# Kernel optimization log

Measured on AMD Instinct MI355X. Metric: run time of the kernel, lower is better.

The kernel has to match this reference:

```python
import jax, jax.numpy as jnp
import numpy as np

NUM_HEADS = 16
D_IN = 1024
D_OUT = 64  # = D_IN // NUM_HEADS
N = 2048


def setup_inputs() -> dict:
    key = jax.random.key(0)
    kx, kq, kk, kv, ko = jax.random.split(key, 5)
    x = jax.random.normal(kx, (N, D_IN), dtype=jnp.float32)
    # per-head projection weights, stacked over heads (torch code keeps a
    # Python list of SelfAttention modules; stacking is the vectorized form)
    q_proj = jax.random.normal(kq, (NUM_HEADS, D_IN, D_OUT), dtype=jnp.float32)
    k_proj = jax.random.normal(kk, (NUM_HEADS, D_IN, D_OUT), dtype=jnp.float32)
    v_proj = jax.random.normal(kv, (NUM_HEADS, D_IN, D_OUT), dtype=jnp.float32)
    o_proj = jax.random.normal(ko, (D_IN, D_IN), dtype=jnp.float32)
    return {"x": x, "q_proj": q_proj, "k_proj": k_proj, "v_proj": v_proj, "o_proj": o_proj}


def reference(x, q_proj, k_proj, v_proj, o_proj):
    d_out = q_proj.shape[-1]
    # per-head projections: [H, N, E]
    q = jnp.einsum('nd,hde->hne', x, q_proj)
    k = jnp.einsum('nd,hde->hne', x, k_proj)
    v = jnp.einsum('nd,hde->hne', x, v_proj)
    # full NxN scores per head (matches the naive torch implementation's math)
    scores = jnp.einsum('hne,hme->hnm', q, k) / jnp.sqrt(jnp.float32(d_out))
    attn = jax.nn.softmax(scores, axis=-1)
    ctx = jnp.einsum('hnm,hme->hne', attn, v)
    # concat heads along the feature dim (head 0 first, as in torch.cat)
    h, n, e = ctx.shape
    out = jnp.transpose(ctx, (1, 0, 2)).reshape(n, h * e)
    return out @ o_proj
```

## Files before the change

### kernel.cpp

```cpp
#include <hip/hip_runtime.h>

#define H 16
#define N 2048
#define E 64
#define D 1024

typedef __attribute__((ext_vector_type(8))) short bf16x8;
typedef __attribute__((ext_vector_type(4))) float f32x4;

__device__ __forceinline__ float bf2f(unsigned short u) {
    union { unsigned int i; float f; } v;
    v.i = ((unsigned int)u) << 16;
    return v.f;
}
__device__ __forceinline__ unsigned short f2bf(float f) {
    unsigned int u = __float_as_uint(f);
    return (unsigned short)((u + 0x7fffu + ((u >> 16) & 1u)) >> 16);
}
#define MFMA(a, b, c) __builtin_amdgcn_mfma_f32_16x16x32_bf16(a, b, c, 0, 0, 0)

typedef __attribute__((address_space(3))) unsigned int lds_u32;
typedef const __attribute__((address_space(1))) unsigned int glb_u32;
__device__ __forceinline__ void dma16(const unsigned short* g, unsigned short* l) {
    __builtin_amdgcn_global_load_lds((glb_u32*)g, (lds_u32*)l, 16, 0, 0);
}

__device__ __forceinline__ int sw8(int row, int c)  { return row * 64  + ((c ^ (row & 7)) << 3); }
__device__ __forceinline__ int sw16(int row, int c) { return row * 128 + ((c ^ (row & 7)) << 3); }

__global__ __launch_bounds__(256) void convert_all_kernel(
    const float* __restrict__ x,
    const float* __restrict__ qw, const float* __restrict__ kw,
    const float* __restrict__ vw, const float* __restrict__ ow,
    unsigned short* __restrict__ xh, unsigned short* __restrict__ xl,
    unsigned short* __restrict__ wBh, unsigned short* __restrict__ wBl,
    unsigned short* __restrict__ wvt, unsigned short* __restrict__ woh)
{
    __shared__ float ts[64][65];
    const int b0 = blockIdx.x;
    const int t = threadIdx.x;
    if (b0 < 2048) {
        const int i = (b0 * 256 + t) * 4;
        const float4 v = *(const float4*)&x[i];
        ushort4 hh, ll;
        hh.x = f2bf(v.x); ll.x = f2bf(v.x - bf2f(hh.x));
        hh.y = f2bf(v.y); ll.y = f2bf(v.y - bf2f(hh.y));
        hh.z = f2bf(v.z); ll.z = f2bf(v.z - bf2f(hh.z));
        hh.w = f2bf(v.w); ll.w = f2bf(v.w - bf2f(hh.w));
        *(ushort4*)&xh[i] = hh;
        *(ushort4*)&xl[i] = ll;
        return;
    }
    const int b = b0 - 2048;
    const float* src;
    int rs, dt, orow0;
    bool has_lo;
    unsigned short *dh, *dl;
    if (b < 768) {
        const int which = b >> 8, r = b & 255, h = r >> 4;
        dt = r & 15;
        src = (which == 0 ? qw : which == 1 ? kw : vw) + ((size_t)h * D + dt * 64) * E;
        rs = E;
        if (which == 0)      { dh = wBh; dl = wBl; orow0 = h * 64;        has_lo = true; }
        else if (which == 1) { dh = wBh; dl = wBl; orow0 = 1024 + h * 64; has_lo = true; }
        else                 { dh = wvt; dl = wBl; orow0 = h * 64;        has_lo = false; }
    } else {
        const int r = b - 768, ct = r >> 4;
        dt = r & 15;
        src = ow + (size_t)(dt * 64) * D + ct * 64;
        rs = D;
        orow0 = ct * 64;
        dh = woh; dl = wBl; has_lo = false;
    }
    {
        const int row = t >> 2, cb = (t & 3) * 16;
        #pragma unroll
        for (int j = 0; j < 16; j += 4) {
            const float4 v = *(const float4*)&src[row * rs + cb + j];
            ts[row][cb + j + 0] = v.x;
            ts[row][cb + j + 1] = v.y;
            ts[row][cb + j + 2] = v.z;
            ts[row][cb + j + 3] = v.w;
        }
    }
    __syncthreads();
    {
        const int cl = t >> 2, dp = (t & 3) * 16;
        bf16x8 hv0, hv1, lv0, lv1;
        #pragma unroll
        for (int i = 0; i < 16; ++i) {
            const float f = ts[dp + i][cl];
            const unsigned short hh = f2bf(f);
            const unsigned short lo = f2bf(f - bf2f(hh));
            if (i < 8) { hv0[i] = (short)hh; lv0[i] = (short)lo; }
            else       { hv1[i - 8] = (short)hh; lv1[i - 8] = (short)lo; }
        }
        const size_t o = (size_t)(orow0 + cl) * D + dt * 64 + dp;
        *(bf16x8*)&dh[o] = hv0;
        *(bf16x8*)&dh[o + 8] = hv1;
        if (has_lo) {
            *(bf16x8*)&dl[o] = lv0;
            *(bf16x8*)&dl[o + 8] = lv1;
        }
    }
}

__global__ __launch_bounds__(256, 3) void qkv_kernel(
    const unsigned short* __restrict__ xh, const unsigned short* __restrict__ xl,
    const unsigned short* __restrict__ wBh, const unsigned short* __restrict__ wBl,
    const unsigned short* __restrict__ wvt,
    unsigned short* __restrict__ Qh, unsigned short* __restrict__ Ql,
    unsigned short* __restrict__ Kh, unsigned short* __restrict__ Kl,
    unsigned short* __restrict__ Vt)
{
    __shared__ unsigned short ash[128 * 64], asl[128 * 64];
    __shared__ unsigned short bsh[64 * 64], bsl[64 * 64];
    const int n0 = blockIdx.x * 128;
    const int ct0 = blockIdx.y;
    const int sec = ct0 >> 4;
    const int hh = ct0 & 15;
    const bool isv = (sec == 2);
    const unsigned short* Bh = isv ? wvt : wBh;
    const size_t brow0 = (sec == 1 ? 1024 : 0) + hh * 64;

    const int t = threadIdx.x;
    const int lane = t & 63, wvi = t >> 6, quad = lane >> 4, l15 = lane & 15;

    f32x4 acc[2][4];
    #pragma unroll
    for (int i = 0; i < 2; ++i)
        #pragma unroll
        for (int j = 0; j < 4; ++j) acc[i][j] = (f32x4){0.f, 0.f, 0.f, 0.f};

    for (int k0 = 0; k0 < D; k0 += 64) {
        __syncthreads();
        #pragma unroll
        for (int p = 0; p < 4; ++p) {
            const int row = p * 32 + wvi * 8 + (lane >> 3);
            const int lc = (lane & 7) ^ (row & 7);
            const int lo = p * 2048 + wvi * 512 + lane * 8;
            const size_t ga = (size_t)(n0 + row) * D + k0 + lc * 8;
            dma16(&xh[ga], &ash[lo]);
            if (!isv) dma16(&xl[ga], &asl[lo]);
        }
        #pragma unroll
        for (int p = 0; p < 2; ++p) {
            const int row = p * 32 + wvi * 8 + (lane >> 3);
            const int lc = (lane & 7) ^ (row & 7);
            const int lo = p * 2048 + wvi * 512 + lane * 8;
            const size_t gb = (brow0 + row) * D + k0 + lc * 8;
            dma16(&Bh[gb], &bsh[lo]);
            if (!isv) dma16(&wBl[gb], &bsl[lo]);
        }
        __syncthreads();

        #pragma unroll
        for (int kwi = 0; kwi < 2; ++kwi) {
            const int c = kwi * 4 + quad;
            bf16x8 ah[2], al[2], bh[4], bl[4];
            #pragma unroll
            for (int i = 0; i < 2; ++i) {
                ah[i] = *(const bf16x8*)&ash[sw8(wvi * 32 + i * 16 + l15, c)];
                if (!isv) al[i] = *(const bf16x8*)&asl[sw8(wvi * 32 + i * 16 + l15, c)];
            }
            #pragma unroll
            for (int j = 0; j < 4; ++j) {
                bh[j] = *(const bf16x8*)&bsh[sw8(j * 16 + l15, c)];
                if (!isv) bl[j] = *(const bf16x8*)&bsl[sw8(j * 16 + l15, c)];
            }
            #pragma unroll
            for (int i = 0; i < 2; ++i)
                #pragma unroll
                for (int j = 0; j < 4; ++j) {
                    acc[i][j] = MFMA(ah[i], bh[j], acc[i][j]);
                    if (!isv) {
                        acc[i][j] = MFMA(ah[i], bl[j], acc[i][j]);
                        acc[i][j] = MFMA(al[i], bh[j], acc[i][j]);
                    }
                }
        }
    }

    if (isv) {
        #pragma unroll
        for (int j = 0; j < 4; ++j) {
            const int e = j * 16 + l15;
            #pragma unroll
            for (int i = 0; i < 2; ++i) {
                const int nb = n0 + wvi * 32 + i * 16 + quad * 4;
                ushort4 pk;
                pk.x = f2bf(acc[i][j][0]);
                pk.y = f2bf(acc[i][j][1]);
                pk.z = f2bf(acc[i][j][2]);
                pk.w = f2bf(acc[i][j][3]);
                *(ushort4*)&Vt[((size_t)hh * 64 + e) * N + nb] = pk;
            }
        }
    } else {
        const float scale = (sec == 0) ? 0.125f : 1.0f;
        unsigned short* Oh = (sec == 0) ? Qh : Kh;
        unsigned short* Ol = (sec == 0) ? Ql : Kl;
        #pragma unroll
        for (int j = 0; j < 4; ++j) {
            const int e = j * 16 + l15;
            #pragma unroll
            for (int i = 0; i < 2; ++i)
                #pragma unroll
                for (int r = 0; r < 4; ++r) {
                    const int n = n0 + wvi * 32 + i * 16 + quad * 4 + r;
                    const float val = acc[i][j][r] * scale;
                    const unsigned short hv = f2bf(val);
                    Oh[((size_t)hh * N + n) * E + e] = hv;
                    Ol[((size_t)hh * N + n) * E + e] = f2bf(val - bf2f(hv));
                }
        }
    }
}

__global__ __launch_bounds__(256, 2) void attn_kernel(
    const unsigned short* __restrict__ Qh, const unsigned short* __restrict__ Ql,
    const unsigned short* __restrict__ Kh, const unsigned short* __restrict__ Kl,
    const unsigned short* __restrict__ Vt,
    unsigned short* __restrict__ Ch)
{
    __shared__ unsigned short ksh[128 * 64], ksl[128 * 64];
    __shared__ unsigned short vts[64 * 128];
    __shared__ unsigned short ps[4 * 16 * 136];
    const int r0 = blockIdx.x * 64, h = blockIdx.y;
    const int t = threadIdx.x, lane = t & 63, wvi = t >> 6, quad = lane >> 4, l15 = lane & 15;

    bf16x8 qfh[2], qfl[2];
    {
        const size_t base = ((size_t)h * N + r0 + wvi * 16 + l15) * E;
        #pragma unroll
        for (int kwi = 0; kwi < 2; ++kwi) {
            qfh[kwi] = *(const bf16x8*)&Qh[base + kwi * 32 + quad * 8];
            qfl[kwi] = *(const bf16x8*)&Ql[base + kwi * 32 + quad * 8];
        }
    }

    f32x4 oacc[4];
    #pragma unroll
    for (int ct = 0; ct < 4; ++ct) oacc[ct] = (f32x4){0.f, 0.f, 0.f, 0.f};
    float mrow[4] = {-1e30f, -1e30f, -1e30f, -1e30f};
    float lrow[4] = {0.f, 0.f, 0.f, 0.f};

    for (int m0 = 0; m0 < N; m0 += 128) {
        __syncthreads();
        #pragma unroll
        for (int p = 0; p < 4; ++p) {
            const int row = p * 32 + wvi * 8 + (lane >> 3);
            const int lc = (lane & 7) ^ (row & 7);
            const int lo = p * 2048 + wvi * 512 + lane * 8;
            const size_t gk = ((size_t)h * N + m0 + row) * E + lc * 8;
            dma16(&Kh[gk], &ksh[lo]);
            dma16(&Kl[gk], &ksl[lo]);
        }
        #pragma unroll
        for (int p = 0; p < 4; ++p) {
            const int row = p * 16 + wvi * 4 + (lane >> 4);
            const int lc = (lane & 15) ^ (row & 7);
            const int lo = p * 2048 + wvi * 512 + lane * 8;
            dma16(&Vt[((size_t)h * 64 + row) * N + m0 + lc * 8], &vts[lo]);
        }
        __syncthreads();

        f32x4 s[8];
        #pragma unroll
        for (int ct = 0; ct < 8; ++ct) s[ct] = (f32x4){0.f, 0.f, 0.f, 0.f};
        #pragma unroll
        for (int kwi = 0; kwi < 2; ++kwi) {
            const int c = kwi * 4 + quad;
            #pragma unroll
            for (int ct = 0; ct < 8; ++ct) {
                const bf16x8 bh = *(const bf16x8*)&ksh[sw8(ct * 16 + l15, c)];
                const bf16x8 bl = *(const bf16x8*)&ksl[sw8(ct * 16 + l15, c)];
                s[ct] = MFMA(qfh[kwi], bh, s[ct]);
                s[ct] = MFMA(qfh[kwi], bl, s[ct]);
                s[ct] = MFMA(qfl[kwi], bh, s[ct]);
            }
        }

        #pragma unroll
        for (int r = 0; r < 4; ++r) {
            float mx = s[0][r];
            #pragma unroll
            for (int ct = 1; ct < 8; ++ct) mx = fmaxf(mx, s[ct][r]);
            mx = fmaxf(mx, __shfl_xor(mx, 1));
            mx = fmaxf(mx, __shfl_xor(mx, 2));
            mx = fmaxf(mx, __shfl_xor(mx, 4));
            mx = fmaxf(mx, __shfl_xor(mx, 8));
            const float mn = fmaxf(mrow[r], mx);
            const float alpha = __expf(mrow[r] - mn);
            mrow[r] = mn;
            float sum = 0.f;
            #pragma unroll
            for (int ct = 0; ct < 8; ++ct) {
                const float p = __expf(s[ct][r] - mn);
                s[ct][r] = p;
                sum += p;
            }
            sum += __shfl_xor(sum, 1);
            sum += __shfl_xor(sum, 2);
            sum += __shfl_xor(sum, 4);
            sum += __shfl_xor(sum, 8);
            lrow[r] = lrow[r] * alpha + sum;
            #pragma unroll
            for (int ct = 0; ct < 4; ++ct) oacc[ct][r] *= alpha;
        }

        #pragma unroll
        for (int ct = 0; ct < 8; ++ct)
            #pragma unroll
            for (int r = 0; r < 4; ++r)
                ps[(wvi * 16 + quad * 4 + r) * 136 + ct * 16 + l15] = f2bf(s[ct][r]);

        #pragma unroll
        for (int kwi = 0; kwi < 4; ++kwi) {
            const bf16x8 pa = *(const bf16x8*)&ps[(wvi * 16 + l15) * 136 + kwi * 32 + quad * 8];
            #pragma unroll
            for (int ct = 0; ct < 4; ++ct) {
                const bf16x8 vb = *(const bf16x8*)&vts[sw16(ct * 16 + l15, kwi * 4 + quad)];
                oacc[ct] = MFMA(pa, vb, oacc[ct]);
            }
        }
    }

    #pragma unroll
    for (int r = 0; r < 4; ++r) {
        const float inv = 1.f / lrow[r];
        const int n = r0 + wvi * 16 + quad * 4 + r;
        #pragma unroll
        for (int ct = 0; ct < 4; ++ct)
            Ch[(size_t)n * D + h * 64 + ct * 16 + l15] = f2bf(oacc[ct][r] * inv);
    }
}

__global__ __launch_bounds__(256, 4) void out_proj_kernel(
    const unsigned short* __restrict__ Chh, const unsigned short* __restrict__ Wh,
    float* __restrict__ out)
{
    __shared__ unsigned short ash[64 * 64], bsh[64 * 64];
    const int n0 = blockIdx.x * 64, c0 = blockIdx.y * 64;
    const int t = threadIdx.x, lane = t & 63, wvi = t >> 6, quad = lane >> 4, l15 = lane & 15;

    f32x4 acc[4];
    #pragma unroll
    for (int j = 0; j < 4; ++j) acc[j] = (f32x4){0.f, 0.f, 0.f, 0.f};

    for (int k0 = 0; k0 < D; k0 += 64) {
        __syncthreads();
        #pragma unroll
        for (int p = 0; p < 2; ++p) {
            const int row = p * 32 + wvi * 8 + (lane >> 3);
            const int lc = (lane & 7) ^ (row & 7);
            const int lo = p * 2048 + wvi * 512 + lane * 8;
            dma16(&Chh[(size_t)(n0 + row) * D + k0 + lc * 8], &ash[lo]);
            dma16(&Wh[(size_t)(c0 + row) * D + k0 + lc * 8], &bsh[lo]);
        }
        __syncthreads();

        #pragma unroll
        for (int kwi = 0; kwi < 2; ++kwi) {
            const int c = kwi * 4 + quad;
            const bf16x8 ah = *(const bf16x8*)&ash[sw8(wvi * 16 + l15, c)];
            #pragma unroll
            for (int j = 0; j < 4; ++j) {
                const bf16x8 bh = *(const bf16x8*)&bsh[sw8(j * 16 + l15, c)];
                acc[j] = MFMA(ah, bh, acc[j]);
            }
        }
    }

    #pragma unroll
    for (int r = 0; r < 4; ++r) {
        const int n = n0 + wvi * 16 + quad * 4 + r;
        #pragma unroll
        for (int j = 0; j < 4; ++j)
            out[(size_t)n * D + c0 + j * 16 + l15] = acc[j][r];
    }
}

extern "C" void kernel_launch(void* const* d_in, const int* in_sizes, int n_in,
                              void* d_out, int out_size, void* d_ws, size_t ws_size,
                              hipStream_t stream) {
    const float* x  = (const float*)d_in[0];
    const float* qw = (const float*)d_in[1];
    const float* kw = (const float*)d_in[2];
    const float* vw = (const float*)d_in[3];
    const float* ow = (const float*)d_in[4];
    float* out = (float*)d_out;

    unsigned short* ws = (unsigned short*)d_ws;
    const size_t M1 = 1024 * 1024;
    unsigned short* wBh = ws;
    unsigned short* wBl = ws + 2 * M1;
    unsigned short* wvt = ws + 4 * M1;
    unsigned short* woh = ws + 5 * M1;
    unsigned short* xh  = ws + 6 * M1;
    unsigned short* xl  = ws + 8 * M1;
    unsigned short* Qh  = ws + 10 * M1;
    unsigned short* Ql  = ws + 12 * M1;
    unsigned short* Kh  = ws + 14 * M1;
    unsigned short* Kl  = ws + 16 * M1;
    unsigned short* Vt  = ws + 18 * M1;
    unsigned short* Ch  = xh;

    convert_all_kernel<<<3072, 256, 0, stream>>>(x, qw, kw, vw, ow,
                                                 xh, xl, wBh, wBl, wvt, woh);
    qkv_kernel<<<dim3(16, 48), 256, 0, stream>>>(xh, xl, wBh, wBl, wvt,
                                                 Qh, Ql, Kh, Kl, Vt);
    attn_kernel<<<dim3(32, 16), 256, 0, stream>>>(Qh, Ql, Kh, Kl, Vt, Ch);
    out_proj_kernel<<<dim3(32, 16), 256, 0, stream>>>(Ch, woh, out);
}
```

Measured before the change: 183.5 us.

## Split attention over KV halves with 128-row Q tiles, double-buffered K, and combine pass

```diff
diff --git a/kernel.cpp b/kernel.cpp
--- a/kernel.cpp
+++ b/kernel.cpp
@@ -27,6 +27,7 @@
 
 __device__ __forceinline__ int sw8(int row, int c)  { return row * 64  + ((c ^ (row & 7)) << 3); }
 __device__ __forceinline__ int sw16(int row, int c) { return row * 128 + ((c ^ (row & 7)) << 3); }
+__device__ __forceinline__ int swp(int row, int c)  { return row * 128 + ((c ^ (row & 15)) << 3); }
 
 __global__ __launch_bounds__(256) void convert_all_kernel(
     const float* __restrict__ x,
@@ -221,53 +222,68 @@
     const unsigned short* __restrict__ Qh, const unsigned short* __restrict__ Ql,
     const unsigned short* __restrict__ Kh, const unsigned short* __restrict__ Kl,
     const unsigned short* __restrict__ Vt,
-    unsigned short* __restrict__ Ch)
+    unsigned short* __restrict__ Op0, unsigned short* __restrict__ Op1,
+    float* __restrict__ mlp)
 {
-    __shared__ unsigned short ksh[128 * 64], ksl[128 * 64];
+    __shared__ unsigned short kbuf[2 * 16384];
     __shared__ unsigned short vts[64 * 128];
-    __shared__ unsigned short ps[4 * 16 * 136];
-    const int r0 = blockIdx.x * 64, h = blockIdx.y;
+    const int r0 = blockIdx.x * 128, h = blockIdx.y, split = blockIdx.z;
+    const int mb = split * 1024;
     const int t = threadIdx.x, lane = t & 63, wvi = t >> 6, quad = lane >> 4, l15 = lane & 15;
 
-    bf16x8 qfh[2], qfl[2];
-    {
-        const size_t base = ((size_t)h * N + r0 + wvi * 16 + l15) * E;
+    bf16x8 qfh[2][2], qfl[2][2];
+    #pragma unroll
+    for (int i = 0; i < 2; ++i) {
+        const size_t base = ((size_t)h * N + r0 + wvi * 32 + i * 16 + l15) * E;
         #pragma unroll
         for (int kwi = 0; kwi < 2; ++kwi) {
-            qfh[kwi] = *(const bf16x8*)&Qh[base + kwi * 32 + quad * 8];
-            qfl[kwi] = *(const bf16x8*)&Ql[base + kwi * 32 + quad * 8];
-        }
-    }
-
-    f32x4 oacc[4];
-    #pragma unroll
-    for (int ct = 0; ct < 4; ++ct) oacc[ct] = (f32x4){0.f, 0.f, 0.f, 0.f};
-    float mrow[4] = {-1e30f, -1e30f, -1e30f, -1e30f};
-    float lrow[4] = {0.f, 0.f, 0.f, 0.f};
-
-    for (int m0 = 0; m0 < N; m0 += 128) {
+            qfh[i][kwi] = *(const bf16x8*)&Qh[base + kwi * 32 + quad * 8];
+            qfl[i][kwi] = *(const bf16x8*)&Ql[base + kwi * 32 + quad * 8];
+        }
+    }
+
+    f32x4 oacc[2][4];
+    float mrow[2][4], lrow[2][4];
+    #pragma unroll
+    for (int i = 0; i < 2; ++i)
+        #pragma unroll
+        for (int j = 0; j < 4; ++j) {
+            oacc[i][j] = (f32x4){0.f, 0.f, 0.f, 0.f};
+            mrow[i][j] = -1e30f;
+            lrow[i][j] = 0.f;
+        }
+
+    #pragma unroll
+    for (int p = 0; p < 4; ++p) {
+        const int row = p * 32 + wvi * 8 + (lane >> 3);
+        const int lc = (lane & 7) ^ (row & 7);
+        const int lo = p * 2048 + wvi * 512 + lane * 8;
+        const size_t gk = ((size_t)h * N + mb + row) * E + lc * 8;
+        dma16(&Kh[gk], &kbuf[lo]);
+        dma16(&Kl[gk], &kbuf[8192 + lo]);
+    }
+
+    for (int it = 0; it < 8; ++it) {
+        const int cur = it & 1;
         __syncthreads();
-        #pragma unroll
-        for (int p = 0; p < 4; ++p) {
-            const int row = p * 32 + wvi * 8 + (lane >> 3);
-            const int lc = (lane & 7) ^ (row & 7);
-            const int lo = p * 2048 + wvi * 512 + lane * 8;
-            const size_t gk = ((size_t)h * N + m0 + row) * E + lc * 8;
-            dma16(&Kh[gk], &ksh[lo]);
-            dma16(&Kl[gk], &ksl[lo]);
-        }
+
         #pragma unroll
         for (int p = 0; p < 4; ++p) {
             const int row = p * 16 + wvi * 4 + (lane >> 4);
             const int lc = (lane & 15) ^ (row & 7);
             const int lo = p * 2048 + wvi * 512 + lane * 8;
-            dma16(&Vt[((size_t)h * 64 + row) * N + m0 + lc * 8], &vts[lo]);
-        }
-        __syncthreads();
-
-        f32x4 s[8];
-        #pragma unroll
-        for (int ct = 0; ct < 8; ++ct) s[ct] = (f32x4){0.f, 0.f, 0.f, 0.f};
+            dma16(&Vt[((size_t)h * 64 + row) * N + mb + it * 128 + lc * 8], &vts[lo]);
+        }
+
+        const unsigned short* ksh = &kbuf[cur * 16384];
+        const unsigned short* ksl = ksh + 8192;
+
+        f32x4 s[2][8];
+        #pragma unroll
+        for (int i = 0; i < 2; ++i)
+            #pragma unroll
+            for (int ct = 0; ct < 8; ++ct) s[i][ct] = (f32x4){0.f, 0.f, 0.f, 0.f};
+
         #pragma unroll
         for (int kwi = 0; kwi < 2; ++kwi) {
             const int c = kwi * 4 + quad;
@@ -275,64 +291,132 @@
             for (int ct = 0; ct < 8; ++ct) {
                 const bf16x8 bh = *(const bf16x8*)&ksh[sw8(ct * 16 + l15, c)];
                 const bf16x8 bl = *(const bf16x8*)&ksl[sw8(ct * 16 + l15, c)];
-                s[ct] = MFMA(qfh[kwi], bh, s[ct]);
-                s[ct] = MFMA(qfh[kwi], bl, s[ct]);
-                s[ct] = MFMA(qfl[kwi], bh, s[ct]);
-            }
-        }
-
+                #pragma unroll
+                for (int i = 0; i < 2; ++i) {
+                    s[i][ct] = MFMA(qfh[i][kwi], bh, s[i][ct]);
+                    s[i][ct] = MFMA(qfh[i][kwi], bl, s[i][ct]);
+                    s[i][ct] = MFMA(qfl[i][kwi], bh, s[i][ct]);
+                }
+            }
+        }
+
+        #pragma unroll
+        for (int i = 0; i < 2; ++i)
+            #pragma unroll
+            for (int r = 0; r < 4; ++r) {
+                float mx = s[i][0][r];
+                #pragma unroll
+                for (int ct = 1; ct < 8; ++ct) mx = fmaxf(mx, s[i][ct][r]);
+                mx = fmaxf(mx, __shfl_xor(mx, 1));
+                mx = fmaxf(mx, __shfl_xor(mx, 2));
+                mx = fmaxf(mx, __shfl_xor(mx, 4));
+                mx = fmaxf(mx, __shfl_xor(mx, 8));
+                const float mn = fmaxf(mrow[i][r], mx);
+                const float alpha = __expf(mrow[i][r] - mn);
+                mrow[i][r] = mn;
+                float sum = 0.f;
+                #pragma unroll
+                for (int ct = 0; ct < 8; ++ct) {
+                    const float p = __expf(s[i][ct][r] - mn);
+                    s[i][ct][r] = p;
+                    sum += p;
+                }
+                sum += __shfl_xor(sum, 1);
+                sum += __shfl_xor(sum, 2);
+                sum += __shfl_xor(sum, 4);
+                sum += __shfl_xor(sum, 8);
+                lrow[i][r] = lrow[i][r] * alpha + sum;
+                #pragma unroll
+                for (int ct = 0; ct < 4; ++ct) oacc[i][ct][r] *= alpha;
+            }
+
+        __syncthreads();
+
+        if (it < 7) {
+            #pragma unroll
+            for (int p = 0; p < 4; ++p) {
+                const int row = p * 32 + wvi * 8 + (lane >> 3);
+                const int lc = (lane & 7) ^ (row & 7);
+                const int lo = (cur ^ 1) * 16384 + p * 2048 + wvi * 512 + lane * 8;
+                const size_t gk = ((size_t)h * N + mb + (it + 1) * 128 + row) * E + lc * 8;
+                dma16(&Kh[gk], &kbuf[lo]);
+                dma16(&Kl[gk], &kbuf[8192 + lo]);
+            }
+        }
+
+        unsigned short* ps = &kbuf[cur * 16384];
+        #pragma unroll
+        for (int i = 0; i < 2; ++i)
+            #pragma unroll
+            for (int ct = 0; ct < 8; ++ct)
+                #pragma unroll
+                for (int r = 0; r < 4; ++r) {
+                    const int row = wvi * 32 + i * 16 + quad * 4 + r;
+                    const int chunk = ct * 2 + (l15 >> 3);
+                    ps[swp(row, chunk) + (l15 & 7)] = f2bf(s[i][ct][r]);
+                }
+
+        #pragma unroll
+        for (int kwi = 0; kwi < 4; ++kwi) {
+            bf16x8 vb[4];
+            #pragma unroll
+            for (int ct = 0; ct < 4; ++ct)
+                vb[ct] = *(const bf16x8*)&vts[sw16(ct * 16 + l15, kwi * 4 + quad)];
+            #pragma unroll
+            for (int i = 0; i < 2; ++i) {
+                const int prow = wvi * 32 + i * 16 + l15;
+                const bf16x8 pa = *(const bf16x8*)&ps[swp(prow, kwi * 4 + quad)];
+                #pragma unroll
+                for (int ct = 0; ct < 4; ++ct)
+                    oacc[i][ct] = MFMA(pa, vb[ct], oacc[i][ct]);
+            }
+        }
+    }
+
+    unsigned short* Opc = split ? Op1 : Op0;
+    #pragma unroll
+    for (int i = 0; i < 2; ++i)
         #pragma unroll
         for (int r = 0; r < 4; ++r) {
-            float mx = s[0][r];
-            #pragma unroll
-            for (int ct = 1; ct < 8; ++ct) mx = fmaxf(mx, s[ct][r]);
-            mx = fmaxf(mx, __shfl_xor(mx, 1));
-            mx = fmaxf(mx, __shfl_xor(mx, 2));
-            mx = fmaxf(mx, __shfl_xor(mx, 4));
-            mx = fmaxf(mx, __shfl_xor(mx, 8));
-            const float mn = fmaxf(mrow[r], mx);
-            const float alpha = __expf(mrow[r] - mn);
-            mrow[r] = mn;
-            float sum = 0.f;
-            #pragma unroll
-            for (int ct = 0; ct < 8; ++ct) {
-                const float p = __expf(s[ct][r] - mn);
-                s[ct][r] = p;
-                sum += p;
-            }
-            sum += __shfl_xor(sum, 1);
-            sum += __shfl_xor(sum, 2);
-            sum += __shfl_xor(sum, 4);
-            sum += __shfl_xor(sum, 8);
-            lrow[r] = lrow[r] * alpha + sum;
-            #pragma unroll
-            for (int ct = 0; ct < 4; ++ct) oacc[ct][r] *= alpha;
-        }
-
-        #pragma unroll
-        for (int ct = 0; ct < 8; ++ct)
-            #pragma unroll
-            for (int r = 0; r < 4; ++r)
-                ps[(wvi * 16 + quad * 4 + r) * 136 + ct * 16 + l15] = f2bf(s[ct][r]);
-
-        #pragma unroll
-        for (int kwi = 0; kwi < 4; ++kwi) {
-            const bf16x8 pa = *(const bf16x8*)&ps[(wvi * 16 + l15) * 136 + kwi * 32 + quad * 8];
-            #pragma unroll
-            for (int ct = 0; ct < 4; ++ct) {
-                const bf16x8 vb = *(const bf16x8*)&vts[sw16(ct * 16 + l15, kwi * 4 + quad)];
-                oacc[ct] = MFMA(pa, vb, oacc[ct]);
-            }
-        }
-    }
-
-    #pragma unroll
-    for (int r = 0; r < 4; ++r) {
-        const float inv = 1.f / lrow[r];
-        const int n = r0 + wvi * 16 + quad * 4 + r;
-        #pragma unroll
-        for (int ct = 0; ct < 4; ++ct)
-            Ch[(size_t)n * D + h * 64 + ct * 16 + l15] = f2bf(oacc[ct][r] * inv);
+            const int n = r0 + wvi * 32 + i * 16 + quad * 4 + r;
+            if (l15 == 0) {
+                mlp[(((size_t)split * 16 + h) * 2048 + n) * 2 + 0] = mrow[i][r];
+                mlp[(((size_t)split * 16 + h) * 2048 + n) * 2 + 1] = lrow[i][r];
+            }
+            #pragma unroll
+            for (int ct = 0; ct < 4; ++ct)
+                Opc[((size_t)h * 2048 + n) * 64 + ct * 16 + l15] = f2bf(oacc[i][ct][r]);
+        }
+}
+
+__global__ __launch_bounds__(256) void combine_kernel(
+    const unsigned short* __restrict__ Op0, const unsigned short* __restrict__ Op1,
+    const float* __restrict__ mlp, unsigned short* __restrict__ Ch)
+{
+    const int h = blockIdx.y;
+    const int n = blockIdx.x * 64 + (threadIdx.x >> 2);
+    const int e0 = (threadIdx.x & 3) * 16;
+    const float m0 = mlp[((size_t)h * 2048 + n) * 2 + 0];
+    const float l0 = mlp[((size_t)h * 2048 + n) * 2 + 1];
+    const float m1 = mlp[((size_t)(16 + h) * 2048 + n) * 2 + 0];
+    const float l1 = mlp[((size_t)(16 + h) * 2048 + n) * 2 + 1];
+    const float M = fmaxf(m0, m1);
+    const float a0 = __expf(m0 - M), a1 = __expf(m1 - M);
+    const float inv = 1.f / (l0 * a0 + l1 * a1);
+    const size_t ib = ((size_t)h * 2048 + n) * 64 + e0;
+    const size_t ob = (size_t)n * D + h * 64 + e0;
+    #pragma unroll
+    for (int j = 0; j < 2; ++j) {
+        const bf16x8 v0 = *(const bf16x8*)&Op0[ib + j * 8];
+        const bf16x8 v1 = *(const bf16x8*)&Op1[ib + j * 8];
+        bf16x8 o;
+        #pragma unroll
+        for (int k = 0; k < 8; ++k) {
+            const float c = (bf2f((unsigned short)v0[k]) * a0 +
+                             bf2f((unsigned short)v1[k]) * a1) * inv;
+            o[k] = (short)f2bf(c);
+        }
+        *(bf16x8*)&Ch[ob + j * 8] = o;
     }
 }
 
@@ -406,10 +490,16 @@
     unsigned short* Vt  = ws + 18 * M1;
     unsigned short* Ch  = xh;
 
+    unsigned short* Op0 = wBh;
+    unsigned short* Op1 = wBl;
+    float* mlp = (float*)wvt;
+
     convert_all_kernel<<<3072, 256, 0, stream>>>(x, qw, kw, vw, ow,
                                                  xh, xl, wBh, wBl, wvt, woh);
     qkv_kernel<<<dim3(16, 48), 256, 0, stream>>>(xh, xl, wBh, wBl, wvt,
                                                  Qh, Ql, Kh, Kl, Vt);
-    attn_kernel<<<dim3(32, 16), 256, 0, stream>>>(Qh, Ql, Kh, Kl, Vt, Ch);
+    attn_kernel<<<dim3(16, 16, 2), 256, 0, stream>>>(Qh, Ql, Kh, Kl, Vt,
+                                                     Op0, Op1, mlp);
+    combine_kernel<<<dim3(32, 16), 256, 0, stream>>>(Op0, Op1, mlp, Ch);
     out_proj_kernel<<<dim3(32, 16), 256, 0, stream>>>(Ch, woh, out);
 }
```

Measured after the change: 181.2 us. Within noise of the previous version (-1.2%).
